# Kernel optimization log

Measured on AMD Instinct MI355X. Metric: run time of the kernel, lower is better.

Reference implementation:

```python
import jax, jax.numpy as jnp
import numpy as np


def _aggregate(x, w, k, pad):
    """Involution-style per-pixel local conv.
    x: [N, C, H, W]; w: [N, heads, wc, k*k, H, W] (stride=1, dilation=1, zero pad).
    Returns [N, heads, C, H, W].
    """
    N, C, H, W = x.shape
    heads, wc = w.shape[1], w.shape[2]
    G = C // wc  # channel groups sharing the same per-pixel weights (c % wc)
    xp = jnp.pad(x, ((0, 0), (0, 0), (pad, pad), (pad, pad)))
    # unfold: [N, C, k*k, H, W] via k*k static shifted slices (no dynamic indexing)
    patches = jnp.stack(
        [xp[:, :, i:i + H, j:j + W] for i in range(k) for j in range(k)], axis=2
    )
    p = patches.reshape(N, G, wc, k * k, H, W)
    # out[n, e, g, v, h, w] = sum_k w[n, e, v, k, h, w] * p[n, g, v, k, h, w]
    out = jnp.einsum('nevkhw,ngvkhw->negvhw', w, p)
    return out.reshape(N, heads, C, H, W)


def reference(x, weight1, weight2):
    out1 = _aggregate(x, weight1, 3, 1)  # 3x3 branch, pad=1
    out2 = _aggregate(x, weight2, 5, 2)  # 5x5 branch, pad=2
    # output layout [N, 2, heads, C, H, W] matching the CUDA index arithmetic
    return jnp.stack([out1, out2], axis=1)


def setup_inputs() -> dict:
    key = jax.random.key(0)
    k1, k2, k3 = jax.random.split(key, 3)
    N, C, H, W = 4, 256, 56, 56
    heads, wc = 1, 32
    x = jax.random.normal(k1, (N, C, H, W), dtype=jnp.float32)
    weight1 = jax.random.normal(k2, (N, heads, wc, 9, H, W), dtype=jnp.float32)
    weight2 = jax.random.normal(k3, (N, heads, wc, 25, H, W), dtype=jnp.float32)
    return {"x": x, "weight1": weight1, "weight2": weight2}
```

## Files before the change

kernel.cpp:

```cpp
#include <hip/hip_runtime.h>


#define N_  4
#define C_  256
#define H_  56
#define W_  56
#define HW_ 3136
#define WC_ 32

#define TILE    14
#define LROWS   18
#define LSTRIDE 68

__global__ __launch_bounds__(256) void lconv_kernel(
    const float* __restrict__ x,
    const float* __restrict__ w1,
    const float* __restrict__ w2,
    float* __restrict__ out)
{
    __shared__ float lds[4 * LROWS * LSTRIDE];

    const int b     = blockIdx.x;
    const int tile  = b & 3;
    const int vlow  = (b >> 2) & 1;
    const int gsel  = (b >> 3) & 1;
    const int vhigh = (b >> 4) & 15;
    const int n     = b >> 8;
    const int v     = (vhigh << 1) | vlow;
    const int r0    = tile * TILE;
    const int nv    = n * WC_ + v;
    const int tid   = threadIdx.x;

    for (int idx = tid; idx < 4 * LROWS * 14; idx += 256) {
        const int c4 = idx % 14;
        const int t2 = idx / 14;
        const int lr = t2 % LROWS;
        const int pl = t2 / LROWS;
        const int gr = r0 - 2 + lr;
        float4 val = make_float4(0.f, 0.f, 0.f, 0.f);
        if (gr >= 0 && gr < H_) {
            const int ch = gsel * 128 + pl * 32 + v;
            val = *(const float4*)(x + (size_t)(n * C_ + ch) * HW_ + gr * W_ + c4 * 4);
        }
        float* lp = &lds[(pl * LROWS + lr) * LSTRIDE + 4 * c4 + 2];
        *(float2*)(lp)     = make_float2(val.x, val.y);
        *(float2*)(lp + 2) = make_float2(val.z, val.w);
    }
    for (int idx = tid; idx < 4 * LROWS * 4; idx += 256) {
        const int k  = idx & 3;
        const int t2 = idx >> 2;
        const int lr = t2 % LROWS;
        const int pl = t2 / LROWS;
        const int slot = (k < 2) ? k : (56 + k);
        lds[(pl * LROWS + lr) * LSTRIDE + slot] = 0.f;
    }
    __syncthreads();

    if (tid >= TILE * 14) return;

    const int row = tid / 14;
    const int s   = tid - row * 14;
    const int wb  = 4 * s;
    const int h   = r0 + row;
    const int hw  = h * W_ + wb;

    const float* w1t = w1 + (size_t)nv * 9  * HW_ + hw;
    const float* w2t = w2 + (size_t)nv * 25 * HW_ + hw;
    const int c0 = gsel * 128 + v;

    float a2[4][4];
    #pragma unroll
    for (int g = 0; g < 4; ++g)
        #pragma unroll
        for (int p = 0; p < 4; ++p) a2[g][p] = 0.f;

    float4 w2r[5][5];
    #pragma unroll
    for (int dj = 0; dj < 5; ++dj)
        w2r[0][dj] = *(const float4*)(w2t + (size_t)dj * HW_);
    #pragma unroll
    for (int dj = 0; dj < 5; ++dj)
        w2r[1][dj] = *(const float4*)(w2t + (size_t)(5 + dj) * HW_);

    float4 w1r[9];
    #pragma unroll
    for (int q = 0; q < 9; ++q)
        w1r[q] = *(const float4*)(w1t + (size_t)q * HW_);

    #pragma unroll
    for (int di = 0; di < 5; ++di) {
        if (di + 2 < 5) {
            #pragma unroll
            for (int dj = 0; dj < 5; ++dj)
                w2r[di + 2][dj] = *(const float4*)(w2t + (size_t)((di + 2) * 5 + dj) * HW_);
        }
        #pragma unroll
        for (int g = 0; g < 4; ++g) {
            const float* lp = &lds[(g * LROWS + row + di) * LSTRIDE + wb];
            const float4 xa  = *(const float4*)(lp);
            const float4 xb4 = *(const float4*)(lp + 4);
            const float xw[8] = {xa.x, xa.y, xa.z, xa.w, xb4.x, xb4.y, xb4.z, xb4.w};
            #pragma unroll
            for (int dj = 0; dj < 5; ++dj) {
                const float* wr = (const float*)&w2r[di][dj];
                #pragma unroll
                for (int p = 0; p < 4; ++p)
                    a2[g][p] += wr[p] * xw[p + dj];
            }
        }
    }

    float* o2 = out + ((size_t)(n * 2 + 1) * C_ + c0) * HW_ + hw;
    #pragma unroll
    for (int g = 0; g < 4; ++g)
        *(float4*)(o2 + (size_t)g * WC_ * HW_) =
            make_float4(a2[g][0], a2[g][1], a2[g][2], a2[g][3]);

    float a1[4][4];
    #pragma unroll
    for (int g = 0; g < 4; ++g)
        #pragma unroll
        for (int p = 0; p < 4; ++p) a1[g][p] = 0.f;

    #pragma unroll
    for (int di = 0; di < 3; ++di) {
        #pragma unroll
        for (int g = 0; g < 4; ++g) {
            const float* lp = &lds[(g * LROWS + row + 1 + di) * LSTRIDE + wb];
            const float4 xa  = *(const float4*)(lp);
            const float4 xb4 = *(const float4*)(lp + 4);
            const float xw[8] = {xa.x, xa.y, xa.z, xa.w, xb4.x, xb4.y, xb4.z, xb4.w};
            #pragma unroll
            for (int dj = 0; dj < 3; ++dj) {
                const float* wr = (const float*)&w1r[di * 3 + dj];
                #pragma unroll
                for (int p = 0; p < 4; ++p)
                    a1[g][p] += wr[p] * xw[p + dj + 1];
            }
        }
    }

    float* o1 = out + ((size_t)(n * 2 + 0) * C_ + c0) * HW_ + hw;
    #pragma unroll
    for (int g = 0; g < 4; ++g)
        *(float4*)(o1 + (size_t)g * WC_ * HW_) =
            make_float4(a1[g][0], a1[g][1], a1[g][2], a1[g][3]);
}

extern "C" void kernel_launch(void* const* d_in, const int* in_sizes, int n_in,
                              void* d_out, int out_size, void* d_ws, size_t ws_size,
                              hipStream_t stream) {
    const float* x  = (const float*)d_in[0];
    const float* w1 = (const float*)d_in[1];
    const float* w2 = (const float*)d_in[2];
    float* out = (float*)d_out;

    dim3 grid(1024), block(256);
    hipLaunchKernelGGL(lconv_kernel, grid, block, 0, stream, x, w1, w2, out);
}
```

Before: 112.3 us.

## Drop LDS staging of input and fuse 3x3 and 5x5 accumulation into one pass

Removes the shared-memory tile of x and its __syncthreads, and has each thread load its input row segments directly from global memory with float4/float2 loads and boundary predicates. The 3x3 branch is merged into the 5x5 row loop so each loaded input row feeds both accumulators, and the two outputs are written together at the end. This avoids LDS traffic and the barrier, but issues redundant global loads of x across threads and rows, leaning on L1/L2 caching. It also holds both accumulator sets live at once, which raises register pressure.

```diff
diff --git a/kernel.cpp b/kernel.cpp
--- a/kernel.cpp
+++ b/kernel.cpp
@@ -8,9 +8,7 @@
 #define HW_ 3136
 #define WC_ 32
 
-#define TILE    14
-#define LROWS   18
-#define LSTRIDE 68
+#define TILE 14
 
 __global__ __launch_bounds__(256) void lconv_kernel(
     const float* __restrict__ x,
@@ -18,8 +16,6 @@
     const float* __restrict__ w2,
     float* __restrict__ out)
 {
-    __shared__ float lds[4 * LROWS * LSTRIDE];
-
     const int b     = blockIdx.x;
     const int tile  = b & 3;
     const int vlow  = (b >> 2) & 1;
@@ -30,31 +26,6 @@
     const int r0    = tile * TILE;
     const int nv    = n * WC_ + v;
     const int tid   = threadIdx.x;
-
-    for (int idx = tid; idx < 4 * LROWS * 14; idx += 256) {
-        const int c4 = idx % 14;
-        const int t2 = idx / 14;
-        const int lr = t2 % LROWS;
-        const int pl = t2 / LROWS;
-        const int gr = r0 - 2 + lr;
-        float4 val = make_float4(0.f, 0.f, 0.f, 0.f);
-        if (gr >= 0 && gr < H_) {
-            const int ch = gsel * 128 + pl * 32 + v;
-            val = *(const float4*)(x + (size_t)(n * C_ + ch) * HW_ + gr * W_ + c4 * 4);
-        }
-        float* lp = &lds[(pl * LROWS + lr) * LSTRIDE + 4 * c4 + 2];
-        *(float2*)(lp)     = make_float2(val.x, val.y);
-        *(float2*)(lp + 2) = make_float2(val.z, val.w);
-    }
-    for (int idx = tid; idx < 4 * LROWS * 4; idx += 256) {
-        const int k  = idx & 3;
-        const int t2 = idx >> 2;
-        const int lr = t2 % LROWS;
-        const int pl = t2 / LROWS;
-        const int slot = (k < 2) ? k : (56 + k);
-        lds[(pl * LROWS + lr) * LSTRIDE + slot] = 0.f;
-    }
-    __syncthreads();
 
     if (tid >= TILE * 14) return;
 
@@ -67,12 +38,13 @@
     const float* w1t = w1 + (size_t)nv * 9  * HW_ + hw;
     const float* w2t = w2 + (size_t)nv * 25 * HW_ + hw;
     const int c0 = gsel * 128 + v;
+    const float* xb = x + (size_t)(n * C_ + c0) * HW_ + wb;
 
-    float a2[4][4];
+    float a2[4][4], a1[4][4];
     #pragma unroll
     for (int g = 0; g < 4; ++g)
         #pragma unroll
-        for (int p = 0; p < 4; ++p) a2[g][p] = 0.f;
+        for (int p = 0; p < 4; ++p) { a2[g][p] = 0.f; a1[g][p] = 0.f; }
 
     float4 w2r[5][5];
     #pragma unroll
@@ -87,6 +59,9 @@
     for (int q = 0; q < 9; ++q)
         w1r[q] = *(const float4*)(w1t + (size_t)q * HW_);
 
+    const bool okL = (s > 0);
+    const bool okR = (s < 13);
+
     #pragma unroll
     for (int di = 0; di < 5; ++di) {
         if (di + 2 < 5) {
@@ -94,12 +69,23 @@
             for (int dj = 0; dj < 5; ++dj)
                 w2r[di + 2][dj] = *(const float4*)(w2t + (size_t)((di + 2) * 5 + dj) * HW_);
         }
+        const int xr    = h - 2 + di;
+        const bool rok  = (xr >= 0) && (xr < H_);
+        const bool do33 = (di >= 1) && (di <= 3);
+
         #pragma unroll
         for (int g = 0; g < 4; ++g) {
-            const float* lp = &lds[(g * LROWS + row + di) * LSTRIDE + wb];
-            const float4 xa  = *(const float4*)(lp);
-            const float4 xb4 = *(const float4*)(lp + 4);
-            const float xw[8] = {xa.x, xa.y, xa.z, xa.w, xb4.x, xb4.y, xb4.z, xb4.w};
+            const float* xp = xb + (size_t)g * WC_ * HW_ + xr * W_;
+            float4 xm = make_float4(0.f, 0.f, 0.f, 0.f);
+            float2 xl = make_float2(0.f, 0.f);
+            float2 xh = make_float2(0.f, 0.f);
+            if (rok) {
+                xm = *(const float4*)(xp);
+                if (okL) xl = *(const float2*)(xp - 2);
+                if (okR) xh = *(const float2*)(xp + 4);
+            }
+            const float xw[8] = {xl.x, xl.y, xm.x, xm.y, xm.z, xm.w, xh.x, xh.y};
+
             #pragma unroll
             for (int dj = 0; dj < 5; ++dj) {
                 const float* wr = (const float*)&w2r[di][dj];
@@ -107,44 +93,26 @@
                 for (int p = 0; p < 4; ++p)
                     a2[g][p] += wr[p] * xw[p + dj];
             }
-        }
-    }
-
-    float* o2 = out + ((size_t)(n * 2 + 1) * C_ + c0) * HW_ + hw;
-    #pragma unroll
-    for (int g = 0; g < 4; ++g)
-        *(float4*)(o2 + (size_t)g * WC_ * HW_) =
-            make_float4(a2[g][0], a2[g][1], a2[g][2], a2[g][3]);
-
-    float a1[4][4];
-    #pragma unroll
-    for (int g = 0; g < 4; ++g)
-        #pragma unroll
-        for (int p = 0; p < 4; ++p) a1[g][p] = 0.f;
-
-    #pragma unroll
-    for (int di = 0; di < 3; ++di) {
-        #pragma unroll
-        for (int g = 0; g < 4; ++g) {
-            const float* lp = &lds[(g * LROWS + row + 1 + di) * LSTRIDE + wb];
-            const float4 xa  = *(const float4*)(lp);
-            const float4 xb4 = *(const float4*)(lp + 4);
-            const float xw[8] = {xa.x, xa.y, xa.z, xa.w, xb4.x, xb4.y, xb4.z, xb4.w};
-            #pragma unroll
-            for (int dj = 0; dj < 3; ++dj) {
-                const float* wr = (const float*)&w1r[di * 3 + dj];
+            if (do33) {
                 #pragma unroll
-                for (int p = 0; p < 4; ++p)
-                    a1[g][p] += wr[p] * xw[p + dj + 1];
+                for (int dj = 0; dj < 3; ++dj) {
+                    const float* wr = (const float*)&w1r[(di - 1) * 3 + dj];
+                    #pragma unroll
+                    for (int p = 0; p < 4; ++p)
+                        a1[g][p] += wr[p] * xw[p + dj + 1];
+                }
             }
         }
     }
 
-    float* o1 = out + ((size_t)(n * 2 + 0) * C_ + c0) * HW_ + hw;
     #pragma unroll
-    for (int g = 0; g < 4; ++g)
-        *(float4*)(o1 + (size_t)g * WC_ * HW_) =
-            make_float4(a1[g][0], a1[g][1], a1[g][2], a1[g][3]);
+    for (int g = 0; g < 4; ++g) {
+        const int ch = c0 + g * WC_;
+        float* o2 = out + ((size_t)(n * 2 + 1) * C_ + ch) * HW_ + hw;
+        float* o1 = out + ((size_t)(n * 2 + 0) * C_ + ch) * HW_ + hw;
+        *(float4*)(o2) = make_float4(a2[g][0], a2[g][1], a2[g][2], a2[g][3]);
+        *(float4*)(o1) = make_float4(a1[g][0], a1[g][1], a1[g][2], a1[g][3]);
+    }
 }
 
 extern "C" void kernel_launch(void* const* d_in, const int* in_sizes, int n_in,
```

New measurement: 126.6 us. +12.8%, slower.
